# Kernel optimization log

Hardware: AMD Instinct MI355X
Metric: run time of the kernel (lower is better)

## Reference

```python
import jax, jax.numpy as jnp
import numpy as np

N = 4            # polynomial points per segment
SEGMENTS = 32
LENGTH = 2.0
HALF = 0.5 * LENGTH
IN_CH = 32
OUT_CH = 32
BATCH = 16
NODES = 1024


def _cheb_points(n):
    # Chebyshev-Lobatto points on [-1, 1] (LagrangePoly basis nodes)
    return -np.cos(np.pi * np.arange(n) / (n - 1))


def setup_inputs() -> dict:
    key = jax.random.key(0)
    k1, k2 = jax.random.split(key)
    x = jax.random.normal(k1, (BATCH, IN_CH, NODES), dtype=jnp.float32)
    # w.data.uniform_(-weight_magnitude, weight_magnitude)
    w = jax.random.uniform(k2, (OUT_CH, IN_CH, (N - 1) * SEGMENTS + 1),
                           dtype=jnp.float32, minval=-1.0, maxval=1.0)
    return {"x": x, "w": w}


def _lagrange_basis(x_in):
    # x_in: [b, c, m] -> basis values [b, c, m, n]
    X = jnp.asarray(_cheb_points(N), dtype=x_in.dtype)
    cols = []
    for j in range(N):
        b = jnp.ones_like(x_in)
        for m in range(N):
            if m != j:
                b = b * (x_in - X[m]) / (X[j] - X[m])
        cols.append(b)
    return jnp.stack(cols, axis=-1)


def reference(x, w):
    # bin index per element, clamped to valid segments
    id_min = jnp.clip(((x + HALF) / LENGTH * SEGMENTS).astype(jnp.int32), 0, SEGMENTS - 1)
    id_max = id_min + 1
    wid_min = id_min * (N - 1)                         # [b, c, m]
    idx = wid_min[..., None] + jnp.arange(N)           # [b, c, m, n]
    c_idx = jnp.arange(IN_CH)[None, :, None, None]     # broadcast channel index
    wg = w[:, c_idx, idx]                              # [o, b, c, m, n] irregular gather
    wg = jnp.transpose(wg, (1, 0, 2, 3, 4))            # [b, o, c, m, n]
    # map x into the local segment coordinate in [-half, half]
    x_min = id_min.astype(x.dtype) / SEGMENTS * 2.0 - 1.0
    x_max = id_max.astype(x.dtype) / SEGMENTS * 2.0 - 1.0
    x_in = LENGTH * (x - x_min) / (x_max - x_min) - HALF
    basis = _lagrange_basis(x_in)                      # [b, c, m, n]
    # sum over in_channels and polynomial points -> [b, o, m]
    return jnp.einsum('bcmj,bocmj->bom', basis, wg)
```

## Files before the change

### kernel.cpp

```cpp
#include <hip/hip_runtime.h>

#define NB 16
#define NC 32
#define NO 32
#define NM 1024
#define SEGS 32
#define WLEN 97
#define MT 16

__global__ __launch_bounds__(256) void repack_w_kernel(const float* __restrict__ w,
                                                       float4* __restrict__ w3) {
    int i = blockIdx.x * blockDim.x + threadIdx.x;
    if (i >= NC * SEGS * NO) return;
    int o   = i & 31;
    int seg = (i >> 5) & 31;
    int c   = i >> 10;
    const float* p = w + (o * NC + c) * WLEN + 3 * seg;
    w3[i] = make_float4(p[0], p[1], p[2], p[3]);
}

__device__ __forceinline__ float4 lagrange_basis(float xv, int& id_out) {
    float v  = (xv + 1.0f) * 16.0f;
    int   id = (int)v;
    id = min(max(id, 0), SEGS - 1);
    const float x_min = (float)id * 0.0625f - 1.0f;
    const float t     = (xv - x_min) * 32.0f - 1.0f;
    const float d0 = t + 1.0f;
    const float d1 = t + 0.5f;
    const float d2 = t - 0.5f;
    const float d3 = t - 1.0f;
    float4 bb;
    bb.x = d1 * d2 * d3 * (-0.66666667f);
    bb.y = d0 * d2 * d3 * ( 1.33333333f);
    bb.z = d0 * d1 * d3 * (-1.33333333f);
    bb.w = d0 * d1 * d2 * ( 0.66666667f);
    id_out = id;
    return bb;
}

__global__ __launch_bounds__(256) void pw_main_kernel(const float* __restrict__ x,
                                                      const float4* __restrict__ w3,
                                                      float* __restrict__ out) {
    const int blk = blockIdx.x;
    const int b   = blk >> 6;
    const int m0  = (blk & 63) * MT;

    __shared__ float4 sb[NC][17];
    __shared__ int    soff[MT][36];

    const int tid = threadIdx.x;

    {
        const int c   = tid >> 3;
        const int mtb = tid & 7;
#pragma unroll
        for (int k = 0; k < 2; ++k) {
            const int mt = mtb + 8 * k;
            const float xv = x[(b * NC + c) * NM + m0 + mt];
            int id;
            float4 bb = lagrange_basis(xv, id);
            sb[c][mt]   = bb;
            soff[mt][c] = (c * SEGS + id) * NO;
        }
    }
    __syncthreads();

    const int lane = tid & 63;
    const int wid  = tid >> 6;
    const int op   = lane & 15;
    const int mt   = wid * 4 + (lane >> 4);

    int4 offs[8];
    {
        const int4* sp = (const int4*)&soff[mt][0];
#pragma unroll
        for (int k = 0; k < 8; ++k) offs[k] = sp[k];
    }

    const float4* __restrict__ wp = w3 + op;

    float acc0 = 0.0f, acc1 = 0.0f;
#pragma unroll
    for (int k = 0; k < 8; ++k) {
        const int4 o4 = offs[k];
#pragma unroll
        for (int j = 0; j < 4; ++j) {
            const int c    = 4 * k + j;
            const int base = (j == 0) ? o4.x : (j == 1) ? o4.y : (j == 2) ? o4.z : o4.w;
            const float4 bb  = sb[c][mt];
            const float4 wv0 = wp[base];
            const float4 wv1 = wp[base + 16];
            acc0 = fmaf(bb.x, wv0.x, acc0);
            acc0 = fmaf(bb.y, wv0.y, acc0);
            acc0 = fmaf(bb.z, wv0.z, acc0);
            acc0 = fmaf(bb.w, wv0.w, acc0);
            acc1 = fmaf(bb.x, wv1.x, acc1);
            acc1 = fmaf(bb.y, wv1.y, acc1);
            acc1 = fmaf(bb.z, wv1.z, acc1);
            acc1 = fmaf(bb.w, wv1.w, acc1);
        }
    }

    out[(b * NO + op) * NM + m0 + mt]        = acc0;
    out[(b * NO + op + 16) * NM + m0 + mt]   = acc1;
}

__global__ __launch_bounds__(256) void pw_fallback_kernel(const float* __restrict__ x,
                                                          const float* __restrict__ w,
                                                          float* __restrict__ out) {
    const int blk = blockIdx.x;
    const int b   = blk >> 7;
    const int m   = (blk & 127) * 8 + (threadIdx.x & 7);
    const int o   = threadIdx.x >> 3;

    float acc = 0.0f;
    for (int c = 0; c < NC; ++c) {
        const float xv = x[(b * NC + c) * NM + m];
        int id;
        float4 bb = lagrange_basis(xv, id);
        const float* p = w + (o * NC + c) * WLEN + 3 * id;
        acc = fmaf(bb.x, p[0], acc);
        acc = fmaf(bb.y, p[1], acc);
        acc = fmaf(bb.z, p[2], acc);
        acc = fmaf(bb.w, p[3], acc);
    }
    out[(b * NO + o) * NM + m] = acc;
}

extern "C" void kernel_launch(void* const* d_in, const int* in_sizes, int n_in,
                              void* d_out, int out_size, void* d_ws, size_t ws_size,
                              hipStream_t stream) {
    const float* x = (const float*)d_in[0];
    const float* w = (const float*)d_in[1];
    float* out = (float*)d_out;

    const size_t w3_bytes = (size_t)NC * SEGS * NO * sizeof(float4);

    if (ws_size >= w3_bytes) {
        float4* w3 = (float4*)d_ws;
        repack_w_kernel<<<(NC * SEGS * NO + 255) / 256, 256, 0, stream>>>(w, w3);
        pw_main_kernel<<<NB * (NM / MT), 256, 0, stream>>>(x, w3, out);
    } else {
        pw_fallback_kernel<<<NB * (NM / 8), 256, 0, stream>>>(x, w, out);
    }
}
```

Baseline: 66.57 us.

## Halve per-block tile to 8 positions, one output channel per thread

Shrinks the m-tile from 16 to 8, doubling the grid to 2048 blocks, and remaps threads so each computes a single output channel for one position instead of two channels. Each thread now issues one float4 gather per input channel instead of two, so a wavefront covers all 32 outputs across two positions. The aim is more parallelism and shorter dependent FMA chains per thread. In exchange the basis staging is repeated across more blocks and each thread does less work to hide latency.

Measured after the change: 68.25 us. +2.5%, slower.

```diff
diff --git a/kernel.cpp b/kernel.cpp
--- a/kernel.cpp
+++ b/kernel.cpp
@@ -6,7 +6,7 @@
 #define NM 1024
 #define SEGS 32
 #define WLEN 97
-#define MT 16
+#define MT 8
 
 __global__ __launch_bounds__(256) void repack_w_kernel(const float* __restrict__ w,
                                                        float4* __restrict__ w3) {
@@ -42,33 +42,27 @@
                                                       const float4* __restrict__ w3,
                                                       float* __restrict__ out) {
     const int blk = blockIdx.x;
-    const int b   = blk >> 6;
-    const int m0  = (blk & 63) * MT;
+    const int b   = blk >> 7;
+    const int m0  = (blk & 127) * MT;
 
-    __shared__ float4 sb[NC][17];
+    __shared__ float4 sb[NC][MT];
     __shared__ int    soff[MT][36];
 
     const int tid = threadIdx.x;
 
     {
-        const int c   = tid >> 3;
-        const int mtb = tid & 7;
-#pragma unroll
-        for (int k = 0; k < 2; ++k) {
-            const int mt = mtb + 8 * k;
-            const float xv = x[(b * NC + c) * NM + m0 + mt];
-            int id;
-            float4 bb = lagrange_basis(xv, id);
-            sb[c][mt]   = bb;
-            soff[mt][c] = (c * SEGS + id) * NO;
-        }
+        const int c  = tid >> 3;
+        const int mt = tid & 7;
+        const float xv = x[(b * NC + c) * NM + m0 + mt];
+        int id;
+        float4 bb = lagrange_basis(xv, id);
+        sb[c][mt]   = bb;
+        soff[mt][c] = (c * SEGS + id) * NO;
     }
     __syncthreads();
 
-    const int lane = tid & 63;
-    const int wid  = tid >> 6;
-    const int op   = lane & 15;
-    const int mt   = wid * 4 + (lane >> 4);
+    const int o  = tid & 31;
+    const int mt = tid >> 5;
 
     int4 offs[8];
     {
@@ -77,9 +71,9 @@
         for (int k = 0; k < 8; ++k) offs[k] = sp[k];
     }
 
-    const float4* __restrict__ wp = w3 + op;
+    const float4* __restrict__ wp = w3 + o;
 
-    float acc0 = 0.0f, acc1 = 0.0f;
+    float acc = 0.0f;
 #pragma unroll
     for (int k = 0; k < 8; ++k) {
         const int4 o4 = offs[k];
@@ -87,22 +81,16 @@
         for (int j = 0; j < 4; ++j) {
             const int c    = 4 * k + j;
             const int base = (j == 0) ? o4.x : (j == 1) ? o4.y : (j == 2) ? o4.z : o4.w;
-            const float4 bb  = sb[c][mt];
-            const float4 wv0 = wp[base];
-            const float4 wv1 = wp[base + 16];
-            acc0 = fmaf(bb.x, wv0.x, acc0);
-            acc0 = fmaf(bb.y, wv0.y, acc0);
-            acc0 = fmaf(bb.z, wv0.z, acc0);
-            acc0 = fmaf(bb.w, wv0.w, acc0);
-            acc1 = fmaf(bb.x, wv1.x, acc1);
-            acc1 = fmaf(bb.y, wv1.y, acc1);
-            acc1 = fmaf(bb.z, wv1.z, acc1);
-            acc1 = fmaf(bb.w, wv1.w, acc1);
+            const float4 bb = sb[c][mt];
+            const float4 wv = wp[base];
+            acc = fmaf(bb.x, wv.x, acc);
+            acc = fmaf(bb.y, wv.y, acc);
+            acc = fmaf(bb.z, wv.z, acc);
+            acc = fmaf(bb.w, wv.w, acc);
         }
     }
 
-    out[(b * NO + op) * NM + m0 + mt]        = acc0;
-    out[(b * NO + op + 16) * NM + m0 + mt]   = acc1;
+    out[(b * NO + o) * NM + m0 + mt] = acc;
 }
 
 __global__ __launch_bounds__(256) void pw_fallback_kernel(const float* __restrict__ x,
```
